# Kernel optimization log

Hardware: AMD Instinct MI355X
Metric: run time of the kernel (lower is better)

Reference implementation:

```python
import jax, jax.numpy as jnp
import numpy as np

B, N, FEAT, D = 8, 2048, 64, 6
RADIUS, NSAMPLE, TOPK, NHEAD, NLAYER = 0.3, 64, 16, 8, 2
EPS = 1e-5


def _bn(x, p, axis=1):
    # eval-mode batchnorm; p rows = (gamma, beta, running_mean, running_var)
    g, b, m, v = p
    sh = [1] * x.ndim
    sh[axis] = -1
    rs = lambda t: t.reshape(sh)
    return (x - rs(m)) * (rs(g) / jnp.sqrt(rs(v) + EPS)) + rs(b)


def _ln(x, g, b):
    mu = jnp.mean(x, -1, keepdims=True)
    var = jnp.mean((x - mu) ** 2, -1, keepdims=True)
    return (x - mu) / jnp.sqrt(var + EPS) * g + b


def _mha(x, w_in, b_in, w_out, b_out):
    bsz, n, e = x.shape
    hd = e // NHEAD
    qkv = x @ w_in.T + b_in                      # [B,N,3E]
    q, k, v = jnp.split(qkv, 3, axis=-1)
    sp = lambda t: t.reshape(bsz, n, NHEAD, hd).transpose(0, 2, 1, 3)  # [B,H,N,hd]
    q, k, v = sp(q), sp(k), sp(v)
    att = jax.nn.softmax(jnp.einsum('bhnd,bhmd->bhnm', q, k) * (1.0 / hd ** 0.5), axis=-1)
    o = jnp.einsum('bhnm,bhmd->bhnd', att, v).transpose(0, 2, 1, 3).reshape(bsz, n, e)
    return o @ w_out.T + b_out


def _forward(sortvec, input, tl_win, tl_bin, tl_wout, tl_bout, tl_w1, tl_b1, tl_w2, tl_b2,
             tl_ln1g, tl_ln1b, tl_ln2g, tl_ln2b,
             fg_w0, fg_b0, fg_w1, fg_b1, fg_w2, fg_b2, fbn0, fbn1, fbn2,
             rc_w0, rc_b0, rc_w1, rc_b1, rc_w2, rc_b2, rbn0, rbn1, rbn2,
             fl_w0, fl_b0, fl_w1, fl_b1, lbn0, lbn1):
    b = sortvec.shape[0]
    n = sortvec.shape[-1]
    relu = jax.nn.relu

    # --- input self-attention (2 post-norm TransformerEncoder layers) ---
    x = sortvec[:, 0].transpose(0, 2, 1)         # [B,N,FEAT]
    for l in range(NLAYER):
        a = _mha(x, tl_win[l], tl_bin[l], tl_wout[l], tl_bout[l])
        x = _ln(x + a, tl_ln1g[l], tl_ln1b[l])
        f = relu(x @ tl_w1[l].T + tl_b1[l]) @ tl_w2[l].T + tl_b2[l]
        x = _ln(x + f, tl_ln2g[l], tl_ln2b[l])

    # --- feat_generator (RFFNet: Conv2d(FEAT,1) then 1x1 convs) + BN + relu ---
    s = jnp.einsum('cf,bnf->bcn', fg_w0, x) + fg_b0[:, None]   # [B,64,N]
    s = relu(_bn(s, fbn0))
    s = relu(_bn(jnp.einsum('co,bon->bcn', fg_w1, s) + fg_b1[:, None], fbn1))
    s = relu(_bn(jnp.einsum('co,bon->bcn', fg_w2, s) + fg_b2[:, None], fbn2))
    scores = s[:, 0]                              # [B,N]

    # --- top-k point selection ---
    _, idx = jax.lax.top_k(scores, TOPK)          # [B,K]
    all_points = input.transpose(0, 2, 1)         # [B,N,6]
    bidx = jnp.arange(b)[:, None]
    query = all_points[bidx, idx]                 # [B,K,6]

    # --- query_ball_point (PointNet++ style) ---
    xyz, qxyz = all_points[..., :3], query[..., :3]
    sqr = jnp.sum((qxyz[:, :, None, :] - xyz[:, None, :, :]) ** 2, -1)   # [B,K,N]
    gidx = jnp.where(sqr > RADIUS ** 2, n, jnp.arange(n)[None, None, :])
    gidx = jnp.sort(gidx, axis=-1)[..., :NSAMPLE]                        # [B,K,S]
    gidx = jnp.where(gidx == n, gidx[..., :1], gidx)
    radius_points = all_points[jnp.arange(b)[:, None, None], gidx]       # [B,K,S,6]
    grouped = jnp.concatenate([query[:, :, None, :], radius_points], axis=2)  # [B,K,S+1,6]

    # --- radius_cnn (Conv3d (1,S+1,6) then 1x1x1) + BN3d + relu ---
    r = jnp.einsum('cpd,bkpd->bck', rc_w0, grouped) + rc_b0[:, None]     # [B,128,K]
    r = relu(_bn(r, rbn0))
    r = relu(_bn(jnp.einsum('co,bok->bck', rc_w1, r) + rc_b1[:, None], rbn1))
    r = relu(_bn(jnp.einsum('co,bok->bck', rc_w2, r) + rc_b2[:, None], rbn2))  # [B,512,K]

    # --- flatten + Linear/BN1d/relu chain ---
    h = r.reshape(b, -1)                          # [B, 512*K]
    h = relu(_bn(h @ fl_w0.T + fl_b0, lbn0))
    h = relu(_bn(h @ fl_w1.T + fl_b1, lbn1))
    return h[..., None], idx                      # [B,512,1], [B,K]


def setup_inputs() -> dict:
    key = jax.random.key(0)
    ks = iter(jax.random.split(key, 80))
    rnd = lambda shape, s=0.02: jax.random.normal(next(ks), shape, jnp.float32) * s

    def bn_p(c):
        g = 1.0 + rnd((c,))
        bb = rnd((c,))
        m = rnd((c,))
        v = 1.0 + 0.1 * jnp.abs(rnd((c,), 1.0))
        return jnp.stack([g, bb, m, v])

    F = FEAT
    return dict(
        sortvec=jax.random.normal(next(ks), (B, 1, F, N), jnp.float32),
        input=jax.random.normal(next(ks), (B, D, N), jnp.float32),
        tl_win=rnd((NLAYER, 3 * F, F)), tl_bin=rnd((NLAYER, 3 * F)),
        tl_wout=rnd((NLAYER, F, F)), tl_bout=rnd((NLAYER, F)),
        tl_w1=rnd((NLAYER, 2048, F)), tl_b1=rnd((NLAYER, 2048)),
        tl_w2=rnd((NLAYER, F, 2048)), tl_b2=rnd((NLAYER, F)),
        tl_ln1g=jnp.ones((NLAYER, F)), tl_ln1b=jnp.zeros((NLAYER, F)),
        tl_ln2g=jnp.ones((NLAYER, F)), tl_ln2b=jnp.zeros((NLAYER, F)),
        fg_w0=rnd((64, F), 0.1), fg_b0=jnp.zeros((64,)),
        fg_w1=rnd((16, 64), 0.1), fg_b1=jnp.zeros((16,)),
        fg_w2=rnd((1, 16), 0.1), fg_b2=jnp.zeros((1,)),
        fbn0=bn_p(64), fbn1=bn_p(16), fbn2=bn_p(1),
        rc_w0=rnd((128, NSAMPLE + 1, D), 0.05), rc_b0=jnp.zeros((128,)),
        rc_w1=rnd((256, 128), 0.05), rc_b1=jnp.zeros((256,)),
        rc_w2=rnd((512, 256), 0.05), rc_b2=jnp.zeros((512,)),
        rbn0=bn_p(128), rbn1=bn_p(256), rbn2=bn_p(512),
        fl_w0=rnd((1024, 512 * TOPK), 0.02), fl_b0=jnp.zeros((1024,)),
        fl_w1=rnd((512, 1024), 0.02), fl_b1=jnp.zeros((512,)),
        lbn0=bn_p(1024), lbn1=bn_p(512),
    )


def reference(sortvec, input, tl_win, tl_bin, tl_wout, tl_bout, tl_w1, tl_b1, tl_w2, tl_b2,
              tl_ln1g, tl_ln1b, tl_ln2g, tl_ln2b,
              fg_w0, fg_b0, fg_w1, fg_b1, fg_w2, fg_b2, fbn0, fbn1, fbn2,
              rc_w0, rc_b0, rc_w1, rc_b1, rc_w2, rc_b2, rbn0, rbn1, rbn2,
              fl_w0, fl_b0, fl_w1, fl_b1, lbn0, lbn1):
    return _forward(sortvec, input, tl_win, tl_bin, tl_wout, tl_bout, tl_w1, tl_b1, tl_w2, tl_b2,
                    tl_ln1g, tl_ln1b, tl_ln2g, tl_ln2b,
                    fg_w0, fg_b0, fg_w1, fg_b1, fg_w2, fg_b2, fbn0, fbn1, fbn2,
                    rc_w0, rc_b0, rc_w1, rc_b1, rc_w2, rc_b2, rbn0, rbn1, rbn2,
                    fl_w0, fl_b0, fl_w1, fl_b1, lbn0, lbn1)
```

## Files before the change

### kernel.cpp

```cpp
#include <hip/hip_runtime.h>
#include <hip/hip_bf16.h>
#include <math.h>

#define BB 8
#define NN 2048
#define FF 64
#define DD 6
#define NSAMP 64
#define TOPK 16
#define NHEAD 8
#define HD 8
#define NLAYER 2
#define EPSF 1e-5f
#define R2 0.09f

typedef short short8 __attribute__((ext_vector_type(8)));
typedef float f32x4 __attribute__((ext_vector_type(4)));
typedef unsigned uint4v __attribute__((ext_vector_type(4)));
typedef unsigned int u32;

__device__ inline unsigned pk2(float x) {
  unsigned b = __float_as_uint(x);
  unsigned hi = (b + 0x7fffu + ((b >> 16) & 1u)) >> 16;
  float r = x - __uint_as_float(hi << 16);
  unsigned c = __float_as_uint(r);
  unsigned lo = (c + 0x7fffu + ((c >> 16) & 1u)) >> 16;
  return (hi << 16) | lo;
}

__device__ inline unsigned short bf16r(float x) {
  unsigned b = __float_as_uint(x);
  return (unsigned short)((b + 0x7fffu + ((b >> 16) & 1u)) >> 16);
}

__device__ __forceinline__ void gl16(const void* g, void* l) {
  __builtin_amdgcn_global_load_lds((const __attribute__((address_space(1))) u32*)g,
                                   (__attribute__((address_space(3))) u32*)l, 16, 0, 0);
}

__global__ void k_transpose(const float* __restrict__ sv, float* __restrict__ x) {
  int i = blockIdx.x * 256 + threadIdx.x;
  if (i >= BB * NN * FF) return;
  int f = i % FF;
  int n = (i / FF) % NN;
  int b = i / (FF * NN);
  x[i] = sv[(b * FF + f) * NN + n];
}

__global__ void k_wpack16(const float* __restrict__ w, unsigned short* __restrict__ hi,
                          unsigned short* __restrict__ lo, int n) {
  int i = blockIdx.x * 256 + threadIdx.x;
  if (i < n) {
    unsigned p = pk2(w[i]);
    hi[i] = (unsigned short)(p >> 16);
    lo[i] = (unsigned short)(p & 0xffffu);
  }
}

__global__ void k_wimg(const float* __restrict__ w1, const float* __restrict__ w2,
                       unsigned short* __restrict__ img) {
  int i = blockIdx.x * 256 + threadIdx.x;
  int e = i & 4095;
  int plane = (i >> 12) & 3;
  int chg = (i >> 14) & 31;
  int l = i >> 19;
  int r = e >> 6, sh = (e >> 3) & 7, inner = e & 7;
  int s = sh ^ (r & 7);
  float v;
  if (plane < 2) v = w1[((size_t)(l * 2048 + chg * 64 + r)) * 64 + s * 8 + inner];
  else           v = w2[((size_t)(l * 64 + r)) * 2048 + chg * 64 + s * 8 + inner];
  unsigned p = pk2(v);
  img[i] = (unsigned short)((plane & 1) ? (p & 0xffffu) : (p >> 16));
}

__global__ void __launch_bounds__(256)
k_qkv4(const float* __restrict__ x, const unsigned short* __restrict__ wqh,
       const unsigned short* __restrict__ wql, const float* __restrict__ bin,
       float* __restrict__ qbuf, uint4* __restrict__ kp4, uint4* __restrict__ vp4) {
  __shared__ __attribute__((aligned(16))) unsigned short l16[64 * 72];
  int row0 = blockIdx.x * 64, y = blockIdx.y, col0 = y * 64;
  int t = threadIdx.x, lane = t & 63, w = t >> 6;
  int nIdx = lane & 15, lq = lane >> 4;
  short8 axh[2], axl[2];
  #pragma unroll
  for (int kbi = 0; kbi < 2; ++kbi) {
    const float* xr = x + (size_t)(row0 + w * 16 + nIdx) * 64 + kbi * 32 + lq * 8;
    #pragma unroll
    for (int j = 0; j < 8; ++j) {
      unsigned p = pk2(xr[j]);
      axh[kbi][j] = (short)(p >> 16);
      axl[kbi][j] = (short)(p & 0xffffu);
    }
  }
  f32x4 acc[4];
  #pragma unroll
  for (int tn = 0; tn < 4; ++tn) acc[tn] = (f32x4){0.f, 0.f, 0.f, 0.f};
  #pragma unroll
  for (int kbi = 0; kbi < 2; ++kbi)
    #pragma unroll
    for (int tn = 0; tn < 4; ++tn) {
      size_t wo = (size_t)(col0 + tn * 16 + nIdx) * 64 + kbi * 32 + lq * 8;
      short8 bh = *(const short8*)(wqh + wo);
      short8 bl = *(const short8*)(wql + wo);
      acc[tn] = __builtin_amdgcn_mfma_f32_16x16x32_bf16(axh[kbi], bh, acc[tn], 0, 0, 0);
      acc[tn] = __builtin_amdgcn_mfma_f32_16x16x32_bf16(axh[kbi], bl, acc[tn], 0, 0, 0);
      acc[tn] = __builtin_amdgcn_mfma_f32_16x16x32_bf16(axl[kbi], bh, acc[tn], 0, 0, 0);
    }
  int b = row0 >> 11, n0 = row0 & (NN - 1);
  if (y == 0) {
    #pragma unroll
    for (int tn = 0; tn < 4; ++tn)
      #pragma unroll
      for (int r = 0; r < 4; ++r) {
        int c = tn * 16 + nIdx;
        qbuf[(size_t)(row0 + w * 16 + lq * 4 + r) * 64 + c] = acc[tn][r] + bin[c];
      }
    return;
  }
  if (y == 1) {
    #pragma unroll
    for (int tn = 0; tn < 4; ++tn)
      #pragma unroll
      for (int r = 0; r < 4; ++r) {
        int c = tn * 16 + nIdx;
        l16[(w * 16 + lq * 4 + r) * 72 + c] = bf16r(acc[tn][r] + bin[64 + c]);
      }
    __syncthreads();
    #pragma unroll
    for (int i = 0; i < 2; ++i) {
      int idx = t + i * 256;
      int h = idx >> 6, tok = idx & 63;
      uint4 v = *(const uint4*)(l16 + tok * 72 + h * 8);
      kp4[(size_t)(b * NHEAD + h) * NN + n0 + tok] = v;
    }
  } else {
    #pragma unroll
    for (int tn = 0; tn < 4; ++tn)
      #pragma unroll
      for (int r = 0; r < 4; ++r) {
        int c = tn * 16 + nIdx;
        l16[c * 72 + (w * 16 + lq * 4 + r)] = bf16r(acc[tn][r] + bin[128 + c]);
      }
    __syncthreads();
    #pragma unroll
    for (int i = 0; i < 2; ++i) {
      int idx = t + i * 256;
      int c = idx >> 3, seg = idx & 7;
      uint4 v = *(const uint4*)(l16 + c * 72 + seg * 8);
      vp4[(size_t)(b * 64 + c) * (NN / 8) + (n0 >> 3) + seg] = v;
    }
  }
}

__global__ void __launch_bounds__(256, 8)
k_attn11(const float* __restrict__ q, const uint4* __restrict__ kp4,
         const unsigned* __restrict__ vp32, float* __restrict__ a) {
  __shared__ uint4 kb4[256];
  __shared__ __attribute__((aligned(16))) unsigned short vb16[9 * 264];
  int t = threadIdx.x;
  int lane = t & 63, w = t >> 6;
  int nIdx = lane & 15, lq = lane >> 4;
  int h = blockIdx.y, b = blockIdx.z;
  int qwb = blockIdx.x * 64 + w * 16;
  int bh = b * NHEAD + h;
  const float kf = 0.35355339059327373f * 1.4426950408889634f;
  short8 qF = {0, 0, 0, 0, 0, 0, 0, 0};
  if (lq == 0) {
    const float* qr = q + ((size_t)(b * NN + qwb + nIdx)) * 64 + h * HD;
    #pragma unroll
    for (int j = 0; j < 8; ++j) qF[j] = (short)bf16r(qr[j] * kf);
  }
  f32x4 acc0 = {0.f, 0.f, 0.f, 0.f};
  f32x4 acc1 = {0.f, 0.f, 0.f, 0.f};
  const uint4* kbase = kp4 + (size_t)bh * NN;
  const unsigned* vbase = vp32 + (size_t)bh * HD * (NN / 2);
  int vn = nIdx < 9 ? nIdx : 8;
  int voff = ((lq & 1) << 2) + ((lq >> 1) << 4);
  if (t < 132) ((unsigned*)(vb16 + 8 * 264))[t] = 0x3f803f80u;
  uint4 kreg = kbase[t];
  unsigned vreg[4];
  #pragma unroll
  for (int i = 0; i < 4; ++i) {
    int g = t + i * 256;
    vreg[i] = vbase[(g >> 7) * (NN / 2) + (g & 127)];
  }
  for (int kc = 0; kc < NN; kc += 256) {
    __syncthreads();
    kb4[t] = kreg;
    #pragma unroll
    for (int i = 0; i < 4; ++i) {
      int g = t + i * 256;
      ((unsigned*)vb16)[(g >> 7) * 132 + (g & 127)] = vreg[i];
    }
    __syncthreads();
    if (kc + 256 < NN) {
      kreg = kbase[kc + 256 + t];
      #pragma unroll
      for (int i = 0; i < 4; ++i) {
        int g = t + i * 256;
        vreg[i] = vbase[(g >> 7) * (NN / 2) + ((kc + 256) >> 1) + (g & 127)];
      }
    }
    #pragma unroll
    for (int s = 0; s < 8; ++s) {
      int kb = s * 32;
      unsigned pk_[4];
      #pragma unroll
      for (int half = 0; half < 2; ++half) {
        int key = kb + half * 16 + nIdx;
        short8 aK = *(const short8*)(kb4 + key);
        f32x4 c = {0.f, 0.f, 0.f, 0.f};
        __builtin_amdgcn_s_setprio(1);
        c = __builtin_amdgcn_mfma_f32_16x16x32_bf16(aK, qF, c, 0, 0, 0);
        __builtin_amdgcn_s_setprio(0);
        float p0 = __builtin_amdgcn_exp2f(c[0]);
        float p1 = __builtin_amdgcn_exp2f(c[1]);
        float p2 = __builtin_amdgcn_exp2f(c[2]);
        float p3 = __builtin_amdgcn_exp2f(c[3]);
        unsigned r0, r1;
        asm("v_cvt_pk_bf16_f32 %0, %1, %2" : "=v"(r0) : "v"(p0), "v"(p1));
        asm("v_cvt_pk_bf16_f32 %0, %1, %2" : "=v"(r1) : "v"(p2), "v"(p3));
        pk_[half * 2]     = r0;
        pk_[half * 2 + 1] = r1;
      }
      unsigned a02 = pk_[0], b02 = pk_[2];
      unsigned a13 = pk_[1], b13 = pk_[3];
      asm("v_permlane32_swap_b32 %0, %1" : "+v"(a02), "+v"(b02));
      asm("v_permlane32_swap_b32 %0, %1" : "+v"(a13), "+v"(b13));
      uint4v bw;
      bw[0] = a02;
      bw[1] = a13;
      bw[2] = b02;
      bw[3] = b13;
      short8 bP = *(short8*)&bw;
      int vo = vn * 264 + kb + voff;
      uint2 v0 = *(const uint2*)(vb16 + vo);
      uint2 v1 = *(const uint2*)(vb16 + vo + 8);
      uint4v av;
      av[0] = v0.x; av[1] = v0.y; av[2] = v1.x; av[3] = v1.y;
      short8 aV = *(short8*)&av;
      __builtin_amdgcn_s_setprio(1);
      if (s & 1) acc1 = __builtin_amdgcn_mfma_f32_16x16x32_bf16(aV, bP, acc1, 0, 0, 0);
      else       acc0 = __builtin_amdgcn_mfma_f32_16x16x32_bf16(aV, bP, acc0, 0, 0, 0);
      __builtin_amdgcn_s_setprio(0);
    }
  }
  f32x4 acc;
  acc[0] = acc0[0] + acc1[0];
  acc[1] = acc0[1] + acc1[1];
  acc[2] = acc0[2] + acc1[2];
  acc[3] = acc0[3] + acc1[3];
  float lr = __shfl(acc[0], 32 + nIdx);
  if (lq < 2) {
    int row = qwb + nIdx;
    float4 o;
    o.x = acc[0] / lr; o.y = acc[1] / lr; o.z = acc[2] / lr; o.w = acc[3] / lr;
    *(float4*)(a + ((size_t)(b * NN + row)) * 64 + h * HD + lq * 4) = o;
  }
}

__global__ void __launch_bounds__(256)
k_proj3(const float* __restrict__ a, const unsigned short* __restrict__ woh,
        const unsigned short* __restrict__ wol, const float* __restrict__ bout,
        const float* __restrict__ g, const float* __restrict__ be,
        float* __restrict__ x) {
  int row0 = blockIdx.x * 64;
  int t = threadIdx.x, lane = t & 63, w = t >> 6;
  int nIdx = lane & 15, lq = lane >> 4;
  short8 axh[2], axl[2];
  #pragma unroll
  for (int kbi = 0; kbi < 2; ++kbi) {
    const float* ar = a + (size_t)(row0 + w * 16 + nIdx) * 64 + kbi * 32 + lq * 8;
    #pragma unroll
    for (int j = 0; j < 8; ++j) {
      unsigned p = pk2(ar[j]);
      axh[kbi][j] = (short)(p >> 16);
      axl[kbi][j] = (short)(p & 0xffffu);
    }
  }
  f32x4 acc[4];
  #pragma unroll
  for (int tn = 0; tn < 4; ++tn) acc[tn] = (f32x4){0.f, 0.f, 0.f, 0.f};
  #pragma unroll
  for (int kbi = 0; kbi < 2; ++kbi)
    #pragma unroll
    for (int tn = 0; tn < 4; ++tn) {
      size_t wo = (size_t)(tn * 16 + nIdx) * 64 + kbi * 32 + lq * 8;
      short8 bh = *(const short8*)(woh + wo);
      short8 bl = *(const short8*)(wol + wo);
      acc[tn] = __builtin_amdgcn_mfma_f32_16x16x32_bf16(axh[kbi], bh, acc[tn], 0, 0, 0);
      acc[tn] = __builtin_amdgcn_mfma_f32_16x16x32_bf16(axh[kbi], bl, acc[tn], 0, 0, 0);
      acc[tn] = __builtin_amdgcn_mfma_f32_16x16x32_bf16(axl[kbi], bh, acc[tn], 0, 0, 0);
    }
  #pragma unroll
  for (int r = 0; r < 4; ++r) {
    int row = row0 + w * 16 + lq * 4 + r;
    float val[4], s = 0.f, sq = 0.f;
    #pragma unroll
    for (int tn = 0; tn < 4; ++tn) {
      int c = tn * 16 + nIdx;
      val[tn] = x[(size_t)row * 64 + c] + bout[c] + acc[tn][r];
      s += val[tn]; sq += val[tn] * val[tn];
    }
    #pragma unroll
    for (int off = 1; off < 16; off <<= 1) { s += __shfl_xor(s, off); sq += __shfl_xor(sq, off); }
    float mean = s * (1.f / 64.f);
    float var = sq * (1.f / 64.f) - mean * mean;
    float rstd = rsqrtf(var + EPSF);
    #pragma unroll
    for (int tn = 0; tn < 4; ++tn) {
      int c = tn * 16 + nIdx;
      x[(size_t)row * 64 + c] = (val[tn] - mean) * rstd * g[c] + be[c];
    }
  }
}

__global__ void __launch_bounds__(256, 2)
k_ffn7(const float* __restrict__ x, const char* __restrict__ img,
       const float* __restrict__ b1, float* __restrict__ part) {
  __shared__ __attribute__((aligned(16))) char W1b[2][16384];
  __shared__ __attribute__((aligned(16))) char W2b[16384];
  __shared__ __attribute__((aligned(16))) unsigned short hpl[2][128 * 64];
  int row0 = blockIdx.x * 128;
  int ks = blockIdx.y, kc = ks * 512;
  int t = threadIdx.x, lane = t & 63, wv = t >> 6;
  int lm = lane & 15, lq = lane >> 4;
  const char* ibase = img + (size_t)ks * 8 * 32768;

  short8 axh[2][2], axl[2][2];
  #pragma unroll
  for (int m = 0; m < 2; ++m)
    #pragma unroll
    for (int kbi = 0; kbi < 2; ++kbi) {
      const float* xr = x + (size_t)(row0 + m * 64 + wv * 16 + lm) * 64 + kbi * 32 + lq * 8;
      #pragma unroll
      for (int j = 0; j < 8; ++j) {
        unsigned p = pk2(xr[j]);
        axh[m][kbi][j] = (short)(p >> 16);
        axl[m][kbi][j] = (short)(p & 0xffffu);
      }
    }
  float bv[8][4];
  #pragma unroll
  for (int ch = 0; ch < 8; ++ch)
    #pragma unroll
    for (int tn = 0; tn < 4; ++tn)
      bv[ch][tn] = b1[kc + ch * 64 + tn * 16 + lm];
  asm volatile("s_waitcnt vmcnt(0)" ::: "memory");
  __builtin_amdgcn_sched_barrier(0);
  #pragma unroll
  for (int i = 0; i < 4; ++i)
    gl16(ibase + i * 4096 + t * 16, &W1b[0][i * 4096 + t * 16]);

  f32x4 acc[2][4];
  #pragma unroll
  for (int m = 0; m < 2; ++m)
    #pragma unroll
    for (int tn = 0; tn < 4; ++tn) acc[m][tn] = (f32x4){0.f, 0.f, 0.f, 0.f};

  #pragma unroll
  for (int ch = 0; ch < 8; ++ch) {
    const int p = ch & 1;
    const char* cbase = ibase + ch * 32768;
    #pragma unroll
    for (int i = 0; i < 4; ++i)
      gl16(cbase + 16384 + i * 4096 + t * 16, &W2b[i * 4096 + t * 16]);
    if (ch < 7) {
      #pragma unroll
      for (int i = 0; i < 4; ++i)
        gl16(cbase + 32768 + i * 4096 + t * 16, &W1b[p ^ 1][i * 4096 + t * 16]);
    }
    if (ch < 7) { asm volatile("s_waitcnt vmcnt(8)" ::: "memory"); }
    else        { asm volatile("s_waitcnt vmcnt(4)" ::: "memory"); }
    __builtin_amdgcn_sched_barrier(0);
    __builtin_amdgcn_s_barrier();
    __builtin_amdgcn_sched_barrier(0);
    const char* P0h = W1b[p];
    const char* P0l = W1b[p] + 8192;
    f32x4 h4[2][4];
    #pragma unroll
    for (int m = 0; m < 2; ++m)
      #pragma unroll
      for (int tn = 0; tn < 4; ++tn) h4[m][tn] = (f32x4){0.f, 0.f, 0.f, 0.f};
    #pragma unroll
    for (int kbi = 0; kbi < 2; ++kbi) {
      int sw = (((kbi * 4 + lq) ^ (lm & 7)) << 4);
      #pragma unroll
      for (int tn = 0; tn < 4; ++tn) {
        int brow = tn * 16 + lm;
        short8 bhi = *(const short8*)(P0h + brow * 128 + sw);
        short8 blo = *(const short8*)(P0l + brow * 128 + sw);
        #pragma unroll
        for (int m = 0; m < 2; ++m) {
          h4[m][tn] = __builtin_amdgcn_mfma_f32_16x16x32_bf16(axh[m][kbi], bhi, h4[m][tn], 0, 0, 0);
          h4[m][tn] = __builtin_amdgcn_mfma_f32_16x16x32_bf16(axh[m][kbi], blo, h4[m][tn], 0, 0, 0);
          h4[m][tn] = __builtin_amdgcn_mfma_f32_16x16x32_bf16(axl[m][kbi], bhi, h4[m][tn], 0, 0, 0);
        }
      }
    }
    #pragma unroll
    for (int m = 0; m < 2; ++m)
      #pragma unroll
      for (int tn = 0; tn < 4; ++tn)
        #pragma unroll
        for (int r = 0; r < 4; ++r) {
          float hv = fmaxf(h4[m][tn][r] + bv[ch][tn], 0.f);
          unsigned u = __float_as_uint(hv);
          float resid = hv - __uint_as_float(u & 0xffff0000u);
          unsigned c2 = __float_as_uint(resid);
          int hrow = m * 64 + wv * 16 + lq * 4 + r, hcol = tn * 16 + lm;
          int off = hrow * 128 + (((hcol >> 3) ^ (hrow & 7)) << 4) + ((hcol & 7) << 1);
          *(unsigned short*)((char*)hpl[0] + off) = (unsigned short)(u >> 16);
          *(unsigned short*)((char*)hpl[1] + off) =
              (unsigned short)((c2 + 0x7fffu + ((c2 >> 16) & 1u)) >> 16);
        }
    if (ch < 7) { asm volatile("s_waitcnt vmcnt(4)" ::: "memory"); }
    else        { asm volatile("s_waitcnt vmcnt(0)" ::: "memory"); }
    __builtin_amdgcn_sched_barrier(0);
    __builtin_amdgcn_s_barrier();
    __builtin_amdgcn_sched_barrier(0);
    const char* P1h = W2b;
    const char* P1l = W2b + 8192;
    #pragma unroll
    for (int kbi = 0; kbi < 2; ++kbi) {
      short8 a2h[2], a2l[2];
      #pragma unroll
      for (int m = 0; m < 2; ++m) {
        int arow = m * 64 + wv * 16 + lm;
        int swa = (((kbi * 4 + lq) ^ (arow & 7)) << 4);
        a2h[m] = *(const short8*)((const char*)hpl[0] + arow * 128 + swa);
        a2l[m] = *(const short8*)((const char*)hpl[1] + arow * 128 + swa);
      }
      int swb = (((kbi * 4 + lq) ^ (lm & 7)) << 4);
      #pragma unroll
      for (int tn = 0; tn < 4; ++tn) {
        int brow = tn * 16 + lm;
        short8 bhi = *(const short8*)(P1h + brow * 128 + swb);
        short8 blo = *(const short8*)(P1l + brow * 128 + swb);
        #pragma unroll
        for (int m = 0; m < 2; ++m) {
          acc[m][tn] = __builtin_amdgcn_mfma_f32_16x16x32_bf16(a2h[m], bhi, acc[m][tn], 0, 0, 0);
          acc[m][tn] = __builtin_amdgcn_mfma_f32_16x16x32_bf16(a2h[m], blo, acc[m][tn], 0, 0, 0);
          acc[m][tn] = __builtin_amdgcn_mfma_f32_16x16x32_bf16(a2l[m], bhi, acc[m][tn], 0, 0, 0);
        }
      }
    }
    __builtin_amdgcn_s_barrier();
    __builtin_amdgcn_sched_barrier(0);
  }
  float* fb = (float*)hpl;
  #pragma unroll
  for (int m = 0; m < 2; ++m)
    #pragma unroll
    for (int tn = 0; tn < 4; ++tn)
      #pragma unroll
      for (int r = 0; r < 4; ++r) {
        int row = m * 64 + wv * 16 + lq * 4 + r;
        int col = (tn * 16 + lm) ^ ((row & 7) << 2);
        fb[row * 64 + col] = acc[m][tn][r];
      }
  __syncthreads();
  float* pb = part + (size_t)ks * (BB * NN * 64);
  #pragma unroll
  for (int i = 0; i < 8; ++i) {
    int idx = t * 4 + i * 1024;
    int row = idx >> 6, c0 = idx & 63;
    int c0s = c0 ^ ((row & 7) << 2);
    float4 v = *(const float4*)(fb + row * 64 + c0s);
    *(float4*)(pb + (size_t)(row0 + row) * 64 + c0) = v;
  }
}

__global__ void k_ffn_ln(const float* __restrict__ part, const float* __restrict__ b2,
                         const float* __restrict__ g, const float* __restrict__ be,
                         float* __restrict__ x) {
  int row = blockIdx.x * 4 + (threadIdx.x >> 6);
  int j = threadIdx.x & 63;
  size_t o = (size_t)row * 64 + j;
  const size_t S = (size_t)BB * NN * 64;
  float val = x[o] + b2[j] + ((part[o] + part[o + S]) + (part[o + 2 * S] + part[o + 3 * S]));
  float s = val;
  for (int off = 32; off; off >>= 1) s += __shfl_xor(s, off);
  s *= (1.f / 64.f);
  float d = val - s;
  float v = d * d;
  for (int off = 32; off; off >>= 1) v += __shfl_xor(v, off);
  v *= (1.f / 64.f);
  x[o] = d * rsqrtf(v + EPSF) * g[j] + be[j];
}

__global__ void k_fg2(const float* __restrict__ x,
                      const float* __restrict__ w0, const float* __restrict__ b0, const float* __restrict__ bn0,
                      const float* __restrict__ w1, const float* __restrict__ b1, const float* __restrict__ bn1,
                      const float* __restrict__ w2, const float* __restrict__ b2, const float* __restrict__ bn2,
                      float* __restrict__ scores) {
  __shared__ float xs[64 * 68];
  __shared__ float ws[64 * 68];
  __shared__ float s0s[64 * 68];
  __shared__ float s1s[64 * 20];
  int row0 = blockIdx.x * 64;
  int t = threadIdx.x;
  #pragma unroll
  for (int i = 0; i < 4; ++i) {
    int q = t + i * 256, r = q >> 4, c = (q & 15) * 4;
    *(float4*)(xs + r * 68 + c) = *(const float4*)(x + (size_t)(row0 + r) * 64 + c);
    *(float4*)(ws + r * 68 + c) = *(const float4*)(w0 + r * 64 + c);
  }
  __syncthreads();
  int tx = t & 15, ty = t >> 4;
  float acc[4][4] = {};
  for (int f = 0; f < 64; f += 4) {
    float4 xv[4], wv[4];
    #pragma unroll
    for (int ri = 0; ri < 4; ++ri) xv[ri] = *(const float4*)(xs + (ty * 4 + ri) * 68 + f);
    #pragma unroll
    for (int ci = 0; ci < 4; ++ci) wv[ci] = *(const float4*)(ws + (tx + 16 * ci) * 68 + f);
    #pragma unroll
    for (int ri = 0; ri < 4; ++ri)
      #pragma unroll
      for (int ci = 0; ci < 4; ++ci)
        acc[ri][ci] += xv[ri].x * wv[ci].x + xv[ri].y * wv[ci].y +
                       xv[ri].z * wv[ci].z + xv[ri].w * wv[ci].w;
  }
  #pragma unroll
  for (int ri = 0; ri < 4; ++ri)
    #pragma unroll
    for (int ci = 0; ci < 4; ++ci) {
      int c = tx + 16 * ci;
      float sc = bn0[c] * rsqrtf(bn0[192 + c] + EPSF);
      float v = (acc[ri][ci] + b0[c] - bn0[128 + c]) * sc + bn0[64 + c];
      s0s[(ty * 4 + ri) * 68 + c] = fmaxf(v, 0.f);
    }
  __syncthreads();
  {
    int rl = t & 63, j0 = t >> 6;
    #pragma unroll
    for (int i = 0; i < 4; ++i) {
      int j = j0 + 4 * i;
      float s = b1[j];
      const float* wr = w1 + j * 64;
      #pragma unroll 16
      for (int c = 0; c < 64; ++c) s += s0s[rl * 68 + c] * wr[c];
      float sc = bn1[j] * rsqrtf(bn1[48 + j] + EPSF);
      s = (s - bn1[32 + j]) * sc + bn1[16 + j];
      s1s[rl * 20 + j] = fmaxf(s, 0.f);
    }
  }
  __syncthreads();
  if (t < 64) {
    float s = b2[0];
    #pragma unroll
    for (int o = 0; o < 16; ++o) s += s1s[t * 20 + o] * w2[o];
    float sc = bn2[0] * rsqrtf(bn2[3] + EPSF);
    s = (s - bn2[2]) * sc + bn2[1];
    scores[row0 + t] = fmaxf(s, 0.f);
  }
}

__global__ void k_topk2(const float* __restrict__ scores, int* __restrict__ idx,
                        float* __restrict__ out_idx) {
  int b = blockIdx.x, t = threadIdx.x;
  float v[8];
  int base = b * NN;
  #pragma unroll
  for (int u = 0; u < 8; ++u) v[u] = scores[base + t + 256 * u];
  __shared__ float wvs[4];
  __shared__ int wis[4];
  __shared__ int winner;
  unsigned taken = 0;
  for (int r = 0; r < TOPK; ++r) {
    float best = -1e30f; int bi = 1 << 30;
    #pragma unroll
    for (int u = 0; u < 8; ++u) {
      if (!((taken >> u) & 1)) {
        float vv = v[u]; int ii = t + 256 * u;
        if (vv > best || (vv == best && ii < bi)) { best = vv; bi = ii; }
      }
    }
    for (int off = 32; off; off >>= 1) {
      float ov = __shfl_xor(best, off);
      int oi = __shfl_xor(bi, off);
      if (ov > best || (ov == best && oi < bi)) { best = ov; bi = oi; }
    }
    if ((t & 63) == 0) { wvs[t >> 6] = best; wis[t >> 6] = bi; }
    __syncthreads();
    if (t == 0) {
      float B = wvs[0]; int I = wis[0];
      #pragma unroll
      for (int q = 1; q < 4; ++q)
        if (wvs[q] > B || (wvs[q] == B && wis[q] < I)) { B = wvs[q]; I = wis[q]; }
      winner = I;
      idx[b * TOPK + r] = I;
      out_idx[b * TOPK + r] = (float)I;
    }
    __syncthreads();
    int w = winner;
    if ((w & 255) == t) taken |= 1u << (w >> 8);
  }
}

__global__ void __launch_bounds__(512)
k_group(const float* __restrict__ inp, const int* __restrict__ idx,
        const float* __restrict__ w0, const float* __restrict__ b0, const float* __restrict__ bn0,
        const float* __restrict__ w1, const float* __restrict__ b1, const float* __restrict__ bn1,
        const float* __restrict__ w2, const float* __restrict__ b2, const float* __restrict__ bn2,
        float* __restrict__ r2g) {
  __shared__ int swave[8 * 64];
  __shared__ int scnt[8];
  __shared__ int gidx[NSAMP];
  __shared__ __attribute__((aligned(16))) float gsh[65 * DD];
  __shared__ __attribute__((aligned(16))) float r0[128];
  __shared__ __attribute__((aligned(16))) float r1[256];
  int k = blockIdx.x, b = blockIdx.y, z = blockIdx.z;
  int t = threadIdx.x;
  int lane = t & 63, w = t >> 6;
  int qn = idx[b * TOPK + k];
  const float* px = inp + (size_t)b * DD * NN;
  float qx = px[qn], qy = px[NN + qn], qz = px[2 * NN + qn];
  {
    int cnt = 0;
    #pragma unroll
    for (int i = 0; i < 4; ++i) {
      int n = w * 256 + i * 64 + lane;
      float dx = px[n] - qx, dy = px[NN + n] - qy, dz = px[2 * NN + n] - qz;
      bool flag = (dx * dx + dy * dy + dz * dz <= R2);
      unsigned long long m = __ballot(flag);
      int pos = cnt + __popcll(m & ((1ull << lane) - 1ull));
      if (flag && pos < NSAMP) swave[w * 64 + pos] = n;
      cnt += (int)__popcll(m);
    }
    if (lane == 0) scnt[w] = cnt < NSAMP ? cnt : NSAMP;
  }
  __syncthreads();
  if (t < NSAMP) {
    int run = 0, val = -1;
    #pragma unroll
    for (int ww = 0; ww < 8; ++ww) {
      int c = scnt[ww];
      int loc = t - run;
      if (loc >= 0 && loc < c) val = swave[ww * 64 + loc];
      run += c;
    }
    gidx[t] = val;
  }
  __syncthreads();
  if (t < NSAMP) {
    int g0 = gidx[0];
    int gt = gidx[t];
    gidx[t] = (gt < 0) ? g0 : gt;
  }
  __syncthreads();
  if (t < 65 * DD) {
    int p = t / DD, d = t - p * DD;
    int n = (p == 0) ? qn : gidx[p - 1];
    gsh[t] = px[d * NN + n];
  }
  __syncthreads();
  {
    int c = t >> 2, part = t & 3;
    const float2* wr = (const float2*)(w0 + c * 390 + part * 98);
    const float2* gr = (const float2*)(gsh + part * 98);
    int n2 = (part == 3) ? 48 : 49;
    float s = 0.f;
    #pragma unroll 7
    for (int i = 0; i < n2; ++i) {
      float2 a = gr[i], ww = wr[i];
      s += a.x * ww.x + a.y * ww.y;
    }
    s += __shfl_xor(s, 1);
    s += __shfl_xor(s, 2);
    if (part == 0) {
      s += b0[c];
      float sc = bn0[c] * rsqrtf(bn0[384 + c] + EPSF);
      s = (s - bn0[256 + c]) * sc + bn0[128 + c];
      r0[c] = fmaxf(s, 0.f);
    }
  }
  __syncthreads();
  {
    int c = t >> 1, part = t & 1;
    const float4* wr = (const float4*)(w1 + c * 128 + part * 64);
    const float4* rr = (const float4*)(r0 + part * 64);
    float s0 = 0.f, s1 = 0.f, s2 = 0.f, s3 = 0.f;
    #pragma unroll 8
    for (int o = 0; o < 16; ++o) {
      float4 a = rr[o], ww = wr[o];
      s0 += a.x * ww.x; s1 += a.y * ww.y; s2 += a.z * ww.z; s3 += a.w * ww.w;
    }
    float s = (s0 + s1) + (s2 + s3);
    s += __shfl_xor(s, 1);
    if (part == 0) {
      s += b1[c];
      float sc = bn1[c] * rsqrtf(bn1[768 + c] + EPSF);
      s = (s - bn1[512 + c]) * sc + bn1[256 + c];
      r1[c] = fmaxf(s, 0.f);
    }
  }
  __syncthreads();
  {
    int c = z * 256 + (t >> 1), part = t & 1;
    const float4* wr = (const float4*)(w2 + c * 256 + part * 128);
    const float4* rr = (const float4*)(r1 + part * 128);
    float s0 = 0.f, s1 = 0.f, s2 = 0.f, s3 = 0.f;
    #pragma unroll 8
    for (int o = 0; o < 32; ++o) {
      float4 a = rr[o], ww = wr[o];
      s0 += a.x * ww.x; s1 += a.y * ww.y; s2 += a.z * ww.z; s3 += a.w * ww.w;
    }
    float s = (s0 + s1) + (s2 + s3);
    s += __shfl_xor(s, 1);
    if (part == 0) {
      s += b2[c];
      float sc = bn2[c] * rsqrtf(bn2[1536 + c] + EPSF);
      s = (s - bn2[1024 + c]) * sc + bn2[512 + c];
      r2g[b * 8192 + c * TOPK + k] = fmaxf(s, 0.f);
    }
  }
}

__global__ void __launch_bounds__(256)
k_fl2(const float* __restrict__ hin, const float* __restrict__ w,
      float* __restrict__ part) {
  __shared__ float hs[8 * 1032];
  int j0 = blockIdx.x * 16;
  int kc = blockIdx.y * 1024;
  int t = threadIdx.x;
  int jj = t >> 4, l = t & 15;
  #pragma unroll
  for (int i = 0; i < 8; ++i) {
    int idx = t + i * 256;
    int b = idx >> 8, off = (idx & 255) * 4;
    *(float4*)(hs + b * 1032 + off) = *(const float4*)(hin + (size_t)b * 8192 + kc + off);
  }
  __syncthreads();
  const float* wr = w + (size_t)(j0 + jj) * 8192 + kc;
  float acc[8] = {};
  #pragma unroll
  for (int k = 0; k < 16; ++k) {
    float4 wv = *(const float4*)(wr + l * 4 + k * 64);
    #pragma unroll
    for (int b = 0; b < 8; ++b) {
      float4 hv = *(const float4*)(hs + b * 1032 + l * 4 + k * 64);
      acc[b] += wv.x * hv.x + wv.y * hv.y + wv.z * hv.z + wv.w * hv.w;
    }
  }
  #pragma unroll
  for (int b = 0; b < 8; ++b) {
    #pragma unroll
    for (int off = 1; off < 16; off <<= 1) acc[b] += __shfl_xor(acc[b], off);
  }
  if (l == 0) {
    #pragma unroll
    for (int b = 0; b < 8; ++b)
      part[((size_t)blockIdx.y * 8 + b) * 1024 + j0 + jj] = acc[b];
  }
}

__global__ void k_flc(const float* __restrict__ part, const float* __restrict__ bias,
                      const float* __restrict__ bn, float* __restrict__ hout) {
  int i = blockIdx.x * 256 + threadIdx.x;
  int b = i >> 10, j = i & 1023;
  float s = bias[j];
  #pragma unroll
  for (int ks = 0; ks < 8; ++ks) s += part[((size_t)ks * 8 + b) * 1024 + j];
  float sc = bn[j] * rsqrtf(bn[3 * 1024 + j] + EPSF);
  s = (s - bn[2 * 1024 + j]) * sc + bn[1024 + j];
  hout[i] = fmaxf(s, 0.f);
}

__global__ void __launch_bounds__(256)
k_fl3(const float* __restrict__ hin, const float* __restrict__ w,
      float* __restrict__ part) {
  __shared__ float hs[8 * 264];
  int j0 = blockIdx.x * 16;
  int kc = blockIdx.y * 256;
  int t = threadIdx.x;
  int jj = t >> 4, l = t & 15;
  #pragma unroll
  for (int i = 0; i < 2; ++i) {
    int idx = t + i * 256;
    int b = idx >> 6, off = (idx & 63) * 4;
    *(float4*)(hs + b * 264 + off) = *(const float4*)(hin + (size_t)b * 1024 + kc + off);
  }
  __syncthreads();
  const float* wr = w + (size_t)(j0 + jj) * 1024 + kc;
  float acc[8] = {};
  #pragma unroll
  for (int k = 0; k < 4; ++k) {
    float4 wv = *(const float4*)(wr + l * 4 + k * 64);
    #pragma unroll
    for (int b = 0; b < 8; ++b) {
      float4 hv = *(const float4*)(hs + b * 264 + l * 4 + k * 64);
      acc[b] += wv.x * hv.x + wv.y * hv.y + wv.z * hv.z + wv.w * hv.w;
    }
  }
  #pragma unroll
  for (int b = 0; b < 8; ++b) {
    #pragma unroll
    for (int off = 1; off < 16; off <<= 1) acc[b] += __shfl_xor(acc[b], off);
  }
  if (l == 0) {
    #pragma unroll
    for (int b = 0; b < 8; ++b)
      part[((size_t)blockIdx.y * 8 + b) * 512 + j0 + jj] = acc[b];
  }
}

__global__ void k_flc2(const float* __restrict__ part, const float* __restrict__ bias,
                       const float* __restrict__ bn, float* __restrict__ hout) {
  int i = blockIdx.x * 256 + threadIdx.x;
  int b = i >> 9, j = i & 511;
  float s = bias[j];
  #pragma unroll
  for (int ks = 0; ks < 4; ++ks) s += part[((size_t)ks * 8 + b) * 512 + j];
  float sc = bn[j] * rsqrtf(bn[3 * 512 + j] + EPSF);
  s = (s - bn[2 * 512 + j]) * sc + bn[512 + j];
  hout[i] = fmaxf(s, 0.f);
}

extern "C" void kernel_launch(void* const* d_in, const int* in_sizes, int n_in,
                              void* d_out, int out_size, void* d_ws, size_t ws_size,
                              hipStream_t stream) {
  const float* sv      = (const float*)d_in[0];
  const float* inp     = (const float*)d_in[1];
  const float* tl_win  = (const float*)d_in[2];
  const float* tl_bin  = (const float*)d_in[3];
  const float* tl_wout = (const float*)d_in[4];
  const float* tl_bout = (const float*)d_in[5];
  const float* tl_w1   = (const float*)d_in[6];
  const float* tl_b1   = (const float*)d_in[7];
  const float* tl_w2   = (const float*)d_in[8];
  const float* tl_b2   = (const float*)d_in[9];
  const float* tl_ln1g = (const float*)d_in[10];
  const float* tl_ln1b = (const float*)d_in[11];
  const float* tl_ln2g = (const float*)d_in[12];
  const float* tl_ln2b = (const float*)d_in[13];
  const float* fg_w0   = (const float*)d_in[14];
  const float* fg_b0   = (const float*)d_in[15];
  const float* fg_w1   = (const float*)d_in[16];
  const float* fg_b1   = (const float*)d_in[17];
  const float* fg_w2   = (const float*)d_in[18];
  const float* fg_b2   = (const float*)d_in[19];
  const float* fbn0    = (const float*)d_in[20];
  const float* fbn1    = (const float*)d_in[21];
  const float* fbn2    = (const float*)d_in[22];
  const float* rc_w0   = (const float*)d_in[23];
  const float* rc_b0   = (const float*)d_in[24];
  const float* rc_w1   = (const float*)d_in[25];
  const float* rc_b1   = (const float*)d_in[26];
  const float* rc_w2   = (const float*)d_in[27];
  const float* rc_b2   = (const float*)d_in[28];
  const float* rbn0    = (const float*)d_in[29];
  const float* rbn1    = (const float*)d_in[30];
  const float* rbn2    = (const float*)d_in[31];
  const float* fl_w0   = (const float*)d_in[32];
  const float* fl_b0   = (const float*)d_in[33];
  const float* fl_w1   = (const float*)d_in[34];
  const float* fl_b1   = (const float*)d_in[35];
  const float* lbn0    = (const float*)d_in[36];
  const float* lbn1    = (const float*)d_in[37];
  (void)in_sizes; (void)n_in; (void)out_size; (void)ws_size;

  float* wsp = (float*)d_ws;
  float* x      = wsp;
  float* qkv    = x + BB * NN * FF;
  float* a      = qkv + BB * NN * 192;
  float* scores = a + BB * NN * FF;
  int*   idxb   = (int*)(scores + BB * NN);
  float* r2g    = (float*)(idxb + BB * TOPK);
  float* h1g    = r2g + BB * 8192;
  unsigned short* img = (unsigned short*)(h1g + BB * 1024);
  unsigned short* wqh = img + (size_t)NLAYER * 32 * 4 * 4096;
  unsigned short* wql = wqh + NLAYER * 192 * 64;
  unsigned short* woh = wql + NLAYER * 192 * 64;
  unsigned short* wol = woh + NLAYER * 64 * 64;
  float* qbuf = qkv;
  unsigned short* kp = (unsigned short*)(qkv + BB * NN * FF);
  unsigned short* vp = kp + (size_t)BB * NHEAD * NN * HD;
  float* part = qkv;
  float* part2 = qkv + 65536;

  float* out = (float*)d_out;

  k_transpose<<<(BB * NN * FF) / 256, 256, 0, stream>>>(sv, x);
  k_wimg<<<(NLAYER * 32 * 4 * 4096) / 256, 256, 0, stream>>>(tl_w1, tl_w2, img);
  k_wpack16<<<(NLAYER * 192 * 64) / 256, 256, 0, stream>>>(tl_win, wqh, wql, NLAYER * 192 * 64);
  k_wpack16<<<(NLAYER * 64 * 64) / 256, 256, 0, stream>>>(tl_wout, woh, wol, NLAYER * 64 * 64);

  for (int l = 0; l < NLAYER; ++l) {
    k_qkv4<<<dim3(BB * NN / 64, 3), 256, 0, stream>>>(x, wqh + l * 192 * 64,
                                                      wql + l * 192 * 64, tl_bin + l * 192,
                                                      qbuf, (uint4*)kp, (uint4*)vp);
    k_attn11<<<dim3(NN / 64, NHEAD, BB), 256, 0, stream>>>(qbuf, (const uint4*)kp,
                                                           (const unsigned*)vp, a);
    k_proj3<<<BB * NN / 64, 256, 0, stream>>>(a, woh + l * 64 * 64, wol + l * 64 * 64,
                                              tl_bout + l * FF,
                                              tl_ln1g + l * FF, tl_ln1b + l * FF, x);
    k_ffn7<<<dim3(BB * NN / 128, 4), 256, 0, stream>>>(x, (const char*)(img + (size_t)l * 524288),
                                                       tl_b1 + l * 2048, part);
    k_ffn_ln<<<BB * NN / 4, 256, 0, stream>>>(part, tl_b2 + l * FF,
                                              tl_ln2g + l * FF, tl_ln2b + l * FF, x);
  }

  k_fg2<<<BB * NN / 64, 256, 0, stream>>>(x, fg_w0, fg_b0, fbn0, fg_w1, fg_b1, fbn1,
                                          fg_w2, fg_b2, fbn2, scores);
  k_topk2<<<BB, 256, 0, stream>>>(scores, idxb, out + BB * 512);
  k_group<<<dim3(TOPK, BB, 2), 512, 0, stream>>>(inp, idxb, rc_w0, rc_b0, rbn0,
                                                 rc_w1, rc_b1, rbn1, rc_w2, rc_b2, rbn2, r2g);
  k_fl2<<<dim3(64, 8), 256, 0, stream>>>(r2g, fl_w0, part);
  k_flc<<<32, 256, 0, stream>>>(part, fl_b0, lbn0, h1g);
  k_fl3<<<dim3(32, 4), 256, 0, stream>>>(h1g, fl_w1, part2);
  k_flc2<<<16, 256, 0, stream>>>(part2, fl_b1, lbn1, out);
}
```

Measured before the change: 413.4 us.

## Fuse prep kernels, raise MFMA wave priority, split group kernel wider

Merges the transpose and three weight-packing kernels into a single prep launch, cutting three kernel launches. Adds s_setprio around the MFMA loops in the FFN kernel so compute waves get issue priority over loaders. Doubles the z-dimension of the group kernel so each thread reduces a quarter of the last layer's dot product, adding parallelism at the cost of more redundant earlier-stage work per block.

```diff
diff --git a/kernel.cpp b/kernel.cpp
--- a/kernel.cpp
+++ b/kernel.cpp
@@ -38,39 +38,43 @@
                                    (__attribute__((address_space(3))) u32*)l, 16, 0, 0);
 }
 
-__global__ void k_transpose(const float* __restrict__ sv, float* __restrict__ x) {
+__global__ void k_prep(const float* __restrict__ sv, float* __restrict__ x,
+                       const float* __restrict__ w1, const float* __restrict__ w2,
+                       unsigned short* __restrict__ img,
+                       const float* __restrict__ win, unsigned short* __restrict__ wqh,
+                       unsigned short* __restrict__ wql,
+                       const float* __restrict__ wout, unsigned short* __restrict__ woh,
+                       unsigned short* __restrict__ wol) {
   int i = blockIdx.x * 256 + threadIdx.x;
-  if (i >= BB * NN * FF) return;
-  int f = i % FF;
-  int n = (i / FF) % NN;
-  int b = i / (FF * NN);
-  x[i] = sv[(b * FF + f) * NN + n];
-}
-
-__global__ void k_wpack16(const float* __restrict__ w, unsigned short* __restrict__ hi,
-                          unsigned short* __restrict__ lo, int n) {
-  int i = blockIdx.x * 256 + threadIdx.x;
-  if (i < n) {
-    unsigned p = pk2(w[i]);
-    hi[i] = (unsigned short)(p >> 16);
-    lo[i] = (unsigned short)(p & 0xffffu);
-  }
-}
-
-__global__ void k_wimg(const float* __restrict__ w1, const float* __restrict__ w2,
-                       unsigned short* __restrict__ img) {
-  int i = blockIdx.x * 256 + threadIdx.x;
-  int e = i & 4095;
-  int plane = (i >> 12) & 3;
-  int chg = (i >> 14) & 31;
-  int l = i >> 19;
-  int r = e >> 6, sh = (e >> 3) & 7, inner = e & 7;
-  int s = sh ^ (r & 7);
-  float v;
-  if (plane < 2) v = w1[((size_t)(l * 2048 + chg * 64 + r)) * 64 + s * 8 + inner];
-  else           v = w2[((size_t)(l * 64 + r)) * 2048 + chg * 64 + s * 8 + inner];
-  unsigned p = pk2(v);
-  img[i] = (unsigned short)((plane & 1) ? (p & 0xffffu) : (p >> 16));
+  {
+    int f = i % FF;
+    int n = (i / FF) % NN;
+    int b = i / (FF * NN);
+    x[i] = sv[(b * FF + f) * NN + n];
+  }
+  {
+    int e = i & 4095;
+    int plane = (i >> 12) & 3;
+    int chg = (i >> 14) & 31;
+    int l = i >> 19;
+    int r = e >> 6, sh = (e >> 3) & 7, inner = e & 7;
+    int s = sh ^ (r & 7);
+    float v;
+    if (plane < 2) v = w1[((size_t)(l * 2048 + chg * 64 + r)) * 64 + s * 8 + inner];
+    else           v = w2[((size_t)(l * 64 + r)) * 2048 + chg * 64 + s * 8 + inner];
+    unsigned p = pk2(v);
+    img[i] = (unsigned short)((plane & 1) ? (p & 0xffffu) : (p >> 16));
+  }
+  if (i < NLAYER * 192 * 64) {
+    unsigned p = pk2(win[i]);
+    wqh[i] = (unsigned short)(p >> 16);
+    wql[i] = (unsigned short)(p & 0xffffu);
+  }
+  if (i < NLAYER * 64 * 64) {
+    unsigned p = pk2(wout[i]);
+    woh[i] = (unsigned short)(p >> 16);
+    wol[i] = (unsigned short)(p & 0xffffu);
+  }
 }
 
 __global__ void __launch_bounds__(256)
@@ -316,7 +320,7 @@
 }
 
 __global__ void __launch_bounds__(256, 2)
-k_ffn7(const float* __restrict__ x, const char* __restrict__ img,
+k_ffn8(const float* __restrict__ x, const char* __restrict__ img,
        const float* __restrict__ b1, float* __restrict__ part) {
   __shared__ __attribute__((aligned(16))) char W1b[2][16384];
   __shared__ __attribute__((aligned(16))) char W2b[16384];
@@ -382,6 +386,7 @@
     for (int m = 0; m < 2; ++m)
       #pragma unroll
       for (int tn = 0; tn < 4; ++tn) h4[m][tn] = (f32x4){0.f, 0.f, 0.f, 0.f};
+    __builtin_amdgcn_s_setprio(1);
     #pragma unroll
     for (int kbi = 0; kbi < 2; ++kbi) {
       int sw = (((kbi * 4 + lq) ^ (lm & 7)) << 4);
@@ -398,6 +403,7 @@
         }
       }
     }
+    __builtin_amdgcn_s_setprio(0);
     #pragma unroll
     for (int m = 0; m < 2; ++m)
       #pragma unroll
@@ -421,6 +427,7 @@
     __builtin_amdgcn_sched_barrier(0);
     const char* P1h = W2b;
     const char* P1l = W2b + 8192;
+    __builtin_amdgcn_s_setprio(1);
     #pragma unroll
     for (int kbi = 0; kbi < 2; ++kbi) {
       short8 a2h[2], a2l[2];
@@ -445,6 +452,7 @@
         }
       }
     }
+    __builtin_amdgcn_s_setprio(0);
     __builtin_amdgcn_s_barrier();
     __builtin_amdgcn_sched_barrier(0);
   }
@@ -698,17 +706,18 @@
   }
   __syncthreads();
   {
-    int c = z * 256 + (t >> 1), part = t & 1;
-    const float4* wr = (const float4*)(w2 + c * 256 + part * 128);
-    const float4* rr = (const float4*)(r1 + part * 128);
+    int c = z * 128 + (t >> 2), part = t & 3;
+    const float4* wr = (const float4*)(w2 + c * 256 + part * 64);
+    const float4* rr = (const float4*)(r1 + part * 64);
     float s0 = 0.f, s1 = 0.f, s2 = 0.f, s3 = 0.f;
     #pragma unroll 8
-    for (int o = 0; o < 32; ++o) {
+    for (int o = 0; o < 16; ++o) {
       float4 a = rr[o], ww = wr[o];
       s0 += a.x * ww.x; s1 += a.y * ww.y; s2 += a.z * ww.z; s3 += a.w * ww.w;
     }
     float s = (s0 + s1) + (s2 + s3);
     s += __shfl_xor(s, 1);
+    s += __shfl_xor(s, 2);
     if (part == 0) {
       s += b2[c];
       float sc = bn2[c] * rsqrtf(bn2[1536 + c] + EPSF);
@@ -882,10 +891,8 @@
 
   float* out = (float*)d_out;
 
-  k_transpose<<<(BB * NN * FF) / 256, 256, 0, stream>>>(sv, x);
-  k_wimg<<<(NLAYER * 32 * 4 * 4096) / 256, 256, 0, stream>>>(tl_w1, tl_w2, img);
-  k_wpack16<<<(NLAYER * 192 * 64) / 256, 256, 0, stream>>>(tl_win, wqh, wql, NLAYER * 192 * 64);
-  k_wpack16<<<(NLAYER * 64 * 64) / 256, 256, 0, stream>>>(tl_wout, woh, wol, NLAYER * 64 * 64);
+  k_prep<<<(BB * NN * FF) / 256, 256, 0, stream>>>(sv, x, tl_w1, tl_w2, img,
+                                                   tl_win, wqh, wql, tl_wout, woh, wol);
 
   for (int l = 0; l < NLAYER; ++l) {
     k_qkv4<<<dim3(BB * NN / 64, 3), 256, 0, stream>>>(x, wqh + l * 192 * 64,
@@ -896,7 +903,7 @@
     k_proj3<<<BB * NN / 64, 256, 0, stream>>>(a, woh + l * 64 * 64, wol + l * 64 * 64,
                                               tl_bout + l * FF,
                                               tl_ln1g + l * FF, tl_ln1b + l * FF, x);
-    k_ffn7<<<dim3(BB * NN / 128, 4), 256, 0, stream>>>(x, (const char*)(img + (size_t)l * 524288),
+    k_ffn8<<<dim3(BB * NN / 128, 4), 256, 0, stream>>>(x, (const char*)(img + (size_t)l * 524288),
                                                        tl_b1 + l * 2048, part);
     k_ffn_ln<<<BB * NN / 4, 256, 0, stream>>>(part, tl_b2 + l * FF,
                                               tl_ln2g + l * FF, tl_ln2b + l * FF, x);
@@ -905,7 +912,7 @@
   k_fg2<<<BB * NN / 64, 256, 0, stream>>>(x, fg_w0, fg_b0, fbn0, fg_w1, fg_b1, fbn1,
                                           fg_w2, fg_b2, fbn2, scores);
   k_topk2<<<BB, 256, 0, stream>>>(scores, idxb, out + BB * 512);
-  k_group<<<dim3(TOPK, BB, 2), 512, 0, stream>>>(inp, idxb, rc_w0, rc_b0, rbn0,
+  k_group<<<dim3(TOPK, BB, 4), 512, 0, stream>>>(inp, idxb, rc_w0, rc_b0, rbn0,
                                                  rc_w1, rc_b1, rbn1, rc_w2, rc_b2, rbn2, r2g);
   k_fl2<<<dim3(64, 8), 256, 0, stream>>>(r2g, fl_w0, part);
   k_flc<<<32, 256, 0, stream>>>(part, fl_b0, lbn0, h1g);
```

Result: no change. 413.6 us (+0.0%).
